# Performance work log

Hardware: AMD Instinct MI355X
Metric: run time of the kernel (lower is better)

## Reference

```python
import jax, jax.numpy as jnp
import numpy as np

R, S, N, D_IN, D_OUT = 4, 8, 4096, 64, 64


def prelu(v, alpha):
    # torch.nn.PReLU with a single learnable slope (default init 0.25)
    return jnp.where(v >= 0, v, alpha * v)


def setup_inputs() -> dict:
    key = jax.random.key(0)
    ks = jax.random.split(key, 6)
    theta = jax.random.uniform(ks[0], (R, S), dtype=jnp.float32)
    t = jax.random.uniform(ks[1], (R, S), dtype=jnp.float32)
    a = jax.random.uniform(ks[2], (R, N, N), dtype=jnp.float32)
    x = jax.random.normal(ks[3], (R, N, D_IN), dtype=jnp.float32)
    # per-relation Linear(input_dim, output_dim): weight [out,in], bias [out]
    fc_w = jax.random.normal(ks[4], (R, D_OUT, D_IN), dtype=jnp.float32) * (1.0 / np.sqrt(D_IN))
    fc_b = jnp.zeros((R, D_OUT), dtype=jnp.float32)
    # Conv2d(R, R, kernel_size=1): weight [R,R,1,1] -> [R,R], bias [R]
    conv_w = jax.random.normal(ks[5], (R, R), dtype=jnp.float32) * (1.0 / np.sqrt(R))
    conv_b = jnp.zeros((R,), dtype=jnp.float32)
    alpha0 = jnp.array(0.25, dtype=jnp.float32)  # PReLU for per-relation activation
    alpha1 = jnp.array(0.25, dtype=jnp.float32)  # PReLU after 1x1 conv
    return dict(theta=theta, t=t, a=a, x=x, fc_w=fc_w, fc_b=fc_b,
                conv_w=conv_w, conv_b=conv_b, alpha0=alpha0, alpha1=alpha1)


def reference(theta, t, a, x, fc_w, fc_b, conv_w, conv_b, alpha0, alpha1):
    # sum_step theta[r,s]*t[r,s]*a[r] == (sum_s theta[r,s]*t[r,s]) * a[r]
    coef = jnp.sum(theta * t, axis=-1)                               # [R]
    # diffusion: scaled dense matmul per relation (scale after matmul to avoid
    # materializing a scaled copy of the NxN matrix)
    feat = coef[:, None, None] * jnp.einsum('rij,rjd->rid', a, x)    # [R,N,D_IN]
    # per-relation Linear + PReLU
    diffusions = prelu(jnp.einsum('rnd,rod->rno', feat, fc_w) + fc_b[:, None, :], alpha0)  # [R,N,D_OUT]
    # 1x1 Conv2d over relation channels + PReLU
    latent = prelu(jnp.einsum('sr,rno->sno', conv_w, diffusions) + conv_b[:, None, None], alpha1)
    return (latent, diffusions)
```

## Files before the change

kernel.cpp:

```cpp
#include <hip/hip_runtime.h>

#define R_ 4
#define S_ 8
#define N_ 4096
#define D_ 64
#define KS_ 128
#define NST_ (N_ / KS_)

typedef __attribute__((ext_vector_type(8))) short bf16x8;
typedef __attribute__((ext_vector_type(4))) float f32x4;

__device__ __forceinline__ unsigned short f2bf(float f) {
    unsigned int u = __float_as_uint(f);
    u = (u + 0x7FFFu + ((u >> 16) & 1u)) >> 16;
    return (unsigned short)u;
}

__device__ __forceinline__ bf16x8 packbf(float4 u, float4 v) {
    bf16x8 f;
    f[0] = (short)f2bf(u.x); f[1] = (short)f2bf(u.y);
    f[2] = (short)f2bf(u.z); f[3] = (short)f2bf(u.w);
    f[4] = (short)f2bf(v.x); f[5] = (short)f2bf(v.y);
    f[6] = (short)f2bf(v.z); f[7] = (short)f2bf(v.w);
    return f;
}

__global__ __launch_bounds__(256) void prep_kernel(
    const float* __restrict__ theta, const float* __restrict__ tt,
    const float* __restrict__ x, const float* __restrict__ fc_w,
    unsigned short* __restrict__ ycombT) {
    int r  = blockIdx.x >> 6;
    int kb = blockIdx.x & 63;
    int tid = threadIdx.x;

    __shared__ float xs[64][64];
    __shared__ float ws[64][65];

    const float* xp = x    + ((size_t)r * N_ + (size_t)kb * 64) * D_;
    const float* wp = fc_w + (size_t)r * D_ * D_;
    for (int i = 0; i < 16; ++i) {
        int flat = i * 256 + tid;
        xs[flat >> 6][flat & 63] = xp[flat];
        ws[flat >> 6][flat & 63] = wp[flat];
    }
    float coef = 0.f;
#pragma unroll
    for (int s = 0; s < S_; ++s) coef += theta[r * S_ + s] * tt[r * S_ + s];
    __syncthreads();

    int o = tid & 63, kg = tid >> 6;
    for (int kl = kg; kl < 64; kl += 4) {
        float dot = 0.f;
#pragma unroll
        for (int d = 0; d < D_; ++d) dot += xs[kl][d] * ws[o][d];
        ycombT[(size_t)(r * D_ + o) * N_ + (size_t)kb * 64 + kl] = f2bf(coef * dot);
    }
}

__global__ __launch_bounds__(512) void gemm_kernel(
    const float* __restrict__ a, const unsigned short* __restrict__ ycombT,
    const float* __restrict__ fc_b, const float* __restrict__ alpha0p,
    float* __restrict__ out) {
    int bid = blockIdx.x;
    int r   = bid & 3;
    int rb  = bid >> 2;
    int tid  = threadIdx.x;
    int wave = tid >> 6;
    int wm   = wave & 3;
    int wk   = wave >> 2;
    int lane = tid & 63;
    int l15  = lane & 15;
    int kg   = lane >> 4;

    __shared__ __align__(16) unsigned short bs[2][64][KS_];
    __shared__ float red[4][16][65];

    int srow = tid >> 3, g2 = (tid & 7) * 2;
    int swz  = (srow & 7) << 1;
    const unsigned short* ysrc = ycombT + (size_t)(r * D_ + srow) * N_ + g2 * 8;

    const float* arow = a + ((size_t)(r * N_ + rb * 64 + wm * 16 + l15)) * N_
                          + wk * 64 + kg * 8;

    f32x4 acc0 = {0.f, 0.f, 0.f, 0.f};
    f32x4 acc1 = {0.f, 0.f, 0.f, 0.f};
    f32x4 acc2 = {0.f, 0.f, 0.f, 0.f};
    f32x4 acc3 = {0.f, 0.f, 0.f, 0.f};

    int swzr = (l15 & 7) << 1;
    int sl0 = ((wk * 8 + 0 + kg) ^ swzr) * 8;
    int sl1 = ((wk * 8 + 4 + kg) ^ swzr) * 8;

    float4 ac0 = *(const float4*)(arow + 0);
    float4 ac1 = *(const float4*)(arow + 4);
    float4 ac2 = *(const float4*)(arow + 32);
    float4 ac3 = *(const float4*)(arow + 36);
    uint4 bv0 = *(const uint4*)(ysrc);
    uint4 bv1 = *(const uint4*)(ysrc + 8);
    *(uint4*)&bs[0][srow][((g2    ) ^ swz) * 8] = bv0;
    *(uint4*)&bs[0][srow][((g2 + 1) ^ swz) * 8] = bv1;
    __syncthreads();
    bv0 = *(const uint4*)(ysrc + KS_);
    bv1 = *(const uint4*)(ysrc + KS_ + 8);
    float4 an0 = *(const float4*)(arow + KS_ + 0);
    float4 an1 = *(const float4*)(arow + KS_ + 4);
    float4 an2 = *(const float4*)(arow + KS_ + 32);
    float4 an3 = *(const float4*)(arow + KS_ + 36);

    for (int s = 0; s < NST_; ++s) {
        int buf = s & 1;
        bf16x8 af0 = packbf(ac0, ac1);
        bf16x8 af1 = packbf(ac2, ac3);
        bf16x8 b00 = *(const bf16x8*)&bs[buf][ 0 + l15][sl0];
        bf16x8 b10 = *(const bf16x8*)&bs[buf][16 + l15][sl0];
        bf16x8 b20 = *(const bf16x8*)&bs[buf][32 + l15][sl0];
        bf16x8 b30 = *(const bf16x8*)&bs[buf][48 + l15][sl0];
        acc0 = __builtin_amdgcn_mfma_f32_16x16x32_bf16(af0, b00, acc0, 0, 0, 0);
        acc1 = __builtin_amdgcn_mfma_f32_16x16x32_bf16(af0, b10, acc1, 0, 0, 0);
        acc2 = __builtin_amdgcn_mfma_f32_16x16x32_bf16(af0, b20, acc2, 0, 0, 0);
        acc3 = __builtin_amdgcn_mfma_f32_16x16x32_bf16(af0, b30, acc3, 0, 0, 0);
        bf16x8 b01 = *(const bf16x8*)&bs[buf][ 0 + l15][sl1];
        bf16x8 b11 = *(const bf16x8*)&bs[buf][16 + l15][sl1];
        bf16x8 b21 = *(const bf16x8*)&bs[buf][32 + l15][sl1];
        bf16x8 b31 = *(const bf16x8*)&bs[buf][48 + l15][sl1];
        acc0 = __builtin_amdgcn_mfma_f32_16x16x32_bf16(af1, b01, acc0, 0, 0, 0);
        acc1 = __builtin_amdgcn_mfma_f32_16x16x32_bf16(af1, b11, acc1, 0, 0, 0);
        acc2 = __builtin_amdgcn_mfma_f32_16x16x32_bf16(af1, b21, acc2, 0, 0, 0);
        acc3 = __builtin_amdgcn_mfma_f32_16x16x32_bf16(af1, b31, acc3, 0, 0, 0);

        ac0 = an0; ac1 = an1; ac2 = an2; ac3 = an3;
        if (s + 2 < NST_) {
            an0 = *(const float4*)(arow + (size_t)(s + 2) * KS_ + 0);
            an1 = *(const float4*)(arow + (size_t)(s + 2) * KS_ + 4);
            an2 = *(const float4*)(arow + (size_t)(s + 2) * KS_ + 32);
            an3 = *(const float4*)(arow + (size_t)(s + 2) * KS_ + 36);
        }
        __syncthreads();
        if (s + 1 < NST_) {
            *(uint4*)&bs[buf ^ 1][srow][((g2    ) ^ swz) * 8] = bv0;
            *(uint4*)&bs[buf ^ 1][srow][((g2 + 1) ^ swz) * 8] = bv1;
            if (s + 2 < NST_) {
                bv0 = *(const uint4*)(ysrc + (size_t)(s + 2) * KS_);
                bv1 = *(const uint4*)(ysrc + (size_t)(s + 2) * KS_ + 8);
            }
            __syncthreads();
        }
    }

    if (wk == 1) {
#pragma unroll
        for (int c = 0; c < 4; ++c) {
            f32x4 acc = (c == 0) ? acc0 : (c == 1) ? acc1 : (c == 2) ? acc2 : acc3;
#pragma unroll
            for (int j = 0; j < 4; ++j)
                red[wm][kg * 4 + j][c * 16 + l15] = acc[j];
        }
    }
    __syncthreads();
    if (wk == 0) {
        const float alpha0 = *alpha0p;
        const size_t diff_off = (size_t)R_ * N_ * D_;
#pragma unroll
        for (int c = 0; c < 4; ++c) {
            f32x4 acc = (c == 0) ? acc0 : (c == 1) ? acc1 : (c == 2) ? acc2 : acc3;
            int col = c * 16 + l15;
            float b = fc_b[r * D_ + col];
#pragma unroll
            for (int j = 0; j < 4; ++j) {
                int rloc = kg * 4 + j;
                float v = acc[j] + red[wm][rloc][col] + b;
                v = (v >= 0.f) ? v : alpha0 * v;
                out[diff_off + ((size_t)(r * N_ + rb * 64 + wm * 16 + rloc)) * D_ + col] = v;
            }
        }
    }
}

__global__ __launch_bounds__(256) void conv_kernel(
    const float* __restrict__ conv_w, const float* __restrict__ conv_b,
    const float* __restrict__ alpha1p, float* __restrict__ out) {
    const size_t nd = (size_t)N_ * D_;
    const size_t diff_off = (size_t)R_ * nd;
    size_t i = ((size_t)blockIdx.x * 256 + threadIdx.x) * 4;

    float4 d0 = *(const float4*)(out + diff_off + 0 * nd + i);
    float4 d1 = *(const float4*)(out + diff_off + 1 * nd + i);
    float4 d2 = *(const float4*)(out + diff_off + 2 * nd + i);
    float4 d3 = *(const float4*)(out + diff_off + 3 * nd + i);
    const float alpha1 = *alpha1p;
#pragma unroll
    for (int s = 0; s < R_; ++s) {
        float w0 = conv_w[s * R_ + 0], w1 = conv_w[s * R_ + 1];
        float w2 = conv_w[s * R_ + 2], w3 = conv_w[s * R_ + 3];
        float cb = conv_b[s];
        float4 v;
        v.x = cb + w0 * d0.x + w1 * d1.x + w2 * d2.x + w3 * d3.x;
        v.y = cb + w0 * d0.y + w1 * d1.y + w2 * d2.y + w3 * d3.y;
        v.z = cb + w0 * d0.z + w1 * d1.z + w2 * d2.z + w3 * d3.z;
        v.w = cb + w0 * d0.w + w1 * d1.w + w2 * d2.w + w3 * d3.w;
        v.x = (v.x >= 0.f) ? v.x : alpha1 * v.x;
        v.y = (v.y >= 0.f) ? v.y : alpha1 * v.y;
        v.z = (v.z >= 0.f) ? v.z : alpha1 * v.z;
        v.w = (v.w >= 0.f) ? v.w : alpha1 * v.w;
        *(float4*)(out + s * nd + i) = v;
    }
}

extern "C" void kernel_launch(void* const* d_in, const int* in_sizes, int n_in,
                              void* d_out, int out_size, void* d_ws, size_t ws_size,
                              hipStream_t stream) {
    const float* theta  = (const float*)d_in[0];
    const float* tt     = (const float*)d_in[1];
    const float* a      = (const float*)d_in[2];
    const float* x      = (const float*)d_in[3];
    const float* fc_w   = (const float*)d_in[4];
    const float* fc_b   = (const float*)d_in[5];
    const float* conv_w = (const float*)d_in[6];
    const float* conv_b = (const float*)d_in[7];
    const float* alpha0 = (const float*)d_in[8];
    const float* alpha1 = (const float*)d_in[9];
    float* out = (float*)d_out;
    unsigned short* ycombT = (unsigned short*)d_ws;

    prep_kernel<<<dim3(R_ * (N_ / 64)), dim3(256), 0, stream>>>(theta, tt, x, fc_w, ycombT);
    gemm_kernel<<<dim3((N_ / 64) * R_), dim3(512), 0, stream>>>(a, ycombT, fc_b, alpha0, out);
    conv_kernel<<<dim3((N_ * D_) / 4 / 256), dim3(256), 0, stream>>>(conv_w, conv_b, alpha1, out);
}
```

Before: 70.59 us.

## Split-K the A@Y GEMM into four partials and fuse reduction with conv epilogue

```diff
diff --git a/kernel.cpp b/kernel.cpp
--- a/kernel.cpp
+++ b/kernel.cpp
@@ -5,7 +5,9 @@
 #define N_ 4096
 #define D_ 64
 #define KS_ 128
-#define NST_ (N_ / KS_)
+#define KQ_ 1024
+#define NST_ (KQ_ / KS_)
+#define PART_ELEMS ((size_t)4 * R_ * N_ * D_)
 
 typedef __attribute__((ext_vector_type(8))) short bf16x8;
 typedef __attribute__((ext_vector_type(4))) float f32x4;
@@ -57,83 +59,101 @@
     }
 }
 
-__global__ __launch_bounds__(512) void gemm_kernel(
+__global__ __launch_bounds__(512, 2) void gemm_kernel(
     const float* __restrict__ a, const unsigned short* __restrict__ ycombT,
-    const float* __restrict__ fc_b, const float* __restrict__ alpha0p,
-    float* __restrict__ out) {
+    float* __restrict__ part) {
     int bid = blockIdx.x;
     int r   = bid & 3;
-    int rb  = bid >> 2;
+    int q   = (bid >> 2) & 3;
+    int rg  = bid >> 4;
     int tid  = threadIdx.x;
     int wave = tid >> 6;
-    int wm   = wave & 3;
-    int wk   = wave >> 2;
     int lane = tid & 63;
     int l15  = lane & 15;
     int kg   = lane >> 4;
 
     __shared__ __align__(16) unsigned short bs[2][64][KS_];
-    __shared__ float red[4][16][65];
 
     int srow = tid >> 3, g2 = (tid & 7) * 2;
     int swz  = (srow & 7) << 1;
-    const unsigned short* ysrc = ycombT + (size_t)(r * D_ + srow) * N_ + g2 * 8;
-
-    const float* arow = a + ((size_t)(r * N_ + rb * 64 + wm * 16 + l15)) * N_
-                          + wk * 64 + kg * 8;
-
-    f32x4 acc0 = {0.f, 0.f, 0.f, 0.f};
-    f32x4 acc1 = {0.f, 0.f, 0.f, 0.f};
-    f32x4 acc2 = {0.f, 0.f, 0.f, 0.f};
-    f32x4 acc3 = {0.f, 0.f, 0.f, 0.f};
+    const unsigned short* ysrc =
+        ycombT + (size_t)(r * D_ + srow) * N_ + (size_t)q * KQ_ + g2 * 8;
+
+    const float* ar0 = a + ((size_t)(r * N_ + rg * 256 + wave * 32 + l15)) * N_
+                         + (size_t)q * KQ_ + kg * 8;
+    const float* ar1 = ar0 + (size_t)16 * N_;
+
+    f32x4 acc[2][4];
+#pragma unroll
+    for (int st = 0; st < 2; ++st)
+#pragma unroll
+        for (int o = 0; o < 4; ++o) acc[st][o] = (f32x4){0.f, 0.f, 0.f, 0.f};
 
     int swzr = (l15 & 7) << 1;
-    int sl0 = ((wk * 8 + 0 + kg) ^ swzr) * 8;
-    int sl1 = ((wk * 8 + 4 + kg) ^ swzr) * 8;
-
-    float4 ac0 = *(const float4*)(arow + 0);
-    float4 ac1 = *(const float4*)(arow + 4);
-    float4 ac2 = *(const float4*)(arow + 32);
-    float4 ac3 = *(const float4*)(arow + 36);
-    uint4 bv0 = *(const uint4*)(ysrc);
-    uint4 bv1 = *(const uint4*)(ysrc + 8);
+
+    float4 an[2][8];
+    bf16x8 af[2][4];
+    uint4 bv0, bv1;
+
+#pragma unroll
+    for (int c = 0; c < 4; ++c) {
+        an[0][2 * c]     = *(const float4*)(ar0 + c * 32);
+        an[0][2 * c + 1] = *(const float4*)(ar0 + c * 32 + 4);
+        an[1][2 * c]     = *(const float4*)(ar1 + c * 32);
+        an[1][2 * c + 1] = *(const float4*)(ar1 + c * 32 + 4);
+    }
+    bv0 = *(const uint4*)(ysrc);
+    bv1 = *(const uint4*)(ysrc + 8);
     *(uint4*)&bs[0][srow][((g2    ) ^ swz) * 8] = bv0;
     *(uint4*)&bs[0][srow][((g2 + 1) ^ swz) * 8] = bv1;
-    __syncthreads();
+#pragma unroll
+    for (int st = 0; st < 2; ++st)
+#pragma unroll
+        for (int c = 0; c < 4; ++c)
+            af[st][c] = packbf(an[st][2 * c], an[st][2 * c + 1]);
+#pragma unroll
+    for (int c = 0; c < 4; ++c) {
+        an[0][2 * c]     = *(const float4*)(ar0 + KS_ + c * 32);
+        an[0][2 * c + 1] = *(const float4*)(ar0 + KS_ + c * 32 + 4);
+        an[1][2 * c]     = *(const float4*)(ar1 + KS_ + c * 32);
+        an[1][2 * c + 1] = *(const float4*)(ar1 + KS_ + c * 32 + 4);
+    }
     bv0 = *(const uint4*)(ysrc + KS_);
     bv1 = *(const uint4*)(ysrc + KS_ + 8);
-    float4 an0 = *(const float4*)(arow + KS_ + 0);
-    float4 an1 = *(const float4*)(arow + KS_ + 4);
-    float4 an2 = *(const float4*)(arow + KS_ + 32);
-    float4 an3 = *(const float4*)(arow + KS_ + 36);
+    __syncthreads();
 
     for (int s = 0; s < NST_; ++s) {
         int buf = s & 1;
-        bf16x8 af0 = packbf(ac0, ac1);
-        bf16x8 af1 = packbf(ac2, ac3);
-        bf16x8 b00 = *(const bf16x8*)&bs[buf][ 0 + l15][sl0];
-        bf16x8 b10 = *(const bf16x8*)&bs[buf][16 + l15][sl0];
-        bf16x8 b20 = *(const bf16x8*)&bs[buf][32 + l15][sl0];
-        bf16x8 b30 = *(const bf16x8*)&bs[buf][48 + l15][sl0];
-        acc0 = __builtin_amdgcn_mfma_f32_16x16x32_bf16(af0, b00, acc0, 0, 0, 0);
-        acc1 = __builtin_amdgcn_mfma_f32_16x16x32_bf16(af0, b10, acc1, 0, 0, 0);
-        acc2 = __builtin_amdgcn_mfma_f32_16x16x32_bf16(af0, b20, acc2, 0, 0, 0);
-        acc3 = __builtin_amdgcn_mfma_f32_16x16x32_bf16(af0, b30, acc3, 0, 0, 0);
-        bf16x8 b01 = *(const bf16x8*)&bs[buf][ 0 + l15][sl1];
-        bf16x8 b11 = *(const bf16x8*)&bs[buf][16 + l15][sl1];
-        bf16x8 b21 = *(const bf16x8*)&bs[buf][32 + l15][sl1];
-        bf16x8 b31 = *(const bf16x8*)&bs[buf][48 + l15][sl1];
-        acc0 = __builtin_amdgcn_mfma_f32_16x16x32_bf16(af1, b01, acc0, 0, 0, 0);
-        acc1 = __builtin_amdgcn_mfma_f32_16x16x32_bf16(af1, b11, acc1, 0, 0, 0);
-        acc2 = __builtin_amdgcn_mfma_f32_16x16x32_bf16(af1, b21, acc2, 0, 0, 0);
-        acc3 = __builtin_amdgcn_mfma_f32_16x16x32_bf16(af1, b31, acc3, 0, 0, 0);
-
-        ac0 = an0; ac1 = an1; ac2 = an2; ac3 = an3;
+#pragma unroll
+        for (int c = 0; c < 4; ++c) {
+            int sl = ((c * 4 + kg) ^ swzr) * 8;
+            bf16x8 b0 = *(const bf16x8*)&bs[buf][ 0 + l15][sl];
+            bf16x8 b1 = *(const bf16x8*)&bs[buf][16 + l15][sl];
+            bf16x8 b2 = *(const bf16x8*)&bs[buf][32 + l15][sl];
+            bf16x8 b3 = *(const bf16x8*)&bs[buf][48 + l15][sl];
+            acc[0][0] = __builtin_amdgcn_mfma_f32_16x16x32_bf16(af[0][c], b0, acc[0][0], 0, 0, 0);
+            acc[0][1] = __builtin_amdgcn_mfma_f32_16x16x32_bf16(af[0][c], b1, acc[0][1], 0, 0, 0);
+            acc[0][2] = __builtin_amdgcn_mfma_f32_16x16x32_bf16(af[0][c], b2, acc[0][2], 0, 0, 0);
+            acc[0][3] = __builtin_amdgcn_mfma_f32_16x16x32_bf16(af[0][c], b3, acc[0][3], 0, 0, 0);
+            acc[1][0] = __builtin_amdgcn_mfma_f32_16x16x32_bf16(af[1][c], b0, acc[1][0], 0, 0, 0);
+            acc[1][1] = __builtin_amdgcn_mfma_f32_16x16x32_bf16(af[1][c], b1, acc[1][1], 0, 0, 0);
+            acc[1][2] = __builtin_amdgcn_mfma_f32_16x16x32_bf16(af[1][c], b2, acc[1][2], 0, 0, 0);
+            acc[1][3] = __builtin_amdgcn_mfma_f32_16x16x32_bf16(af[1][c], b3, acc[1][3], 0, 0, 0);
+        }
+#pragma unroll
+        for (int st = 0; st < 2; ++st)
+#pragma unroll
+            for (int c = 0; c < 4; ++c)
+                af[st][c] = packbf(an[st][2 * c], an[st][2 * c + 1]);
         if (s + 2 < NST_) {
-            an0 = *(const float4*)(arow + (size_t)(s + 2) * KS_ + 0);
-            an1 = *(const float4*)(arow + (size_t)(s + 2) * KS_ + 4);
-            an2 = *(const float4*)(arow + (size_t)(s + 2) * KS_ + 32);
-            an3 = *(const float4*)(arow + (size_t)(s + 2) * KS_ + 36);
+            size_t ko = (size_t)(s + 2) * KS_;
+#pragma unroll
+            for (int c = 0; c < 4; ++c) {
+                an[0][2 * c]     = *(const float4*)(ar0 + ko + c * 32);
+                an[0][2 * c + 1] = *(const float4*)(ar0 + ko + c * 32 + 4);
+                an[1][2 * c]     = *(const float4*)(ar1 + ko + c * 32);
+                an[1][2 * c + 1] = *(const float4*)(ar1 + ko + c * 32 + 4);
+            }
         }
         __syncthreads();
         if (s + 1 < NST_) {
@@ -147,62 +167,60 @@
         }
     }
 
-    if (wk == 1) {
-#pragma unroll
-        for (int c = 0; c < 4; ++c) {
-            f32x4 acc = (c == 0) ? acc0 : (c == 1) ? acc1 : (c == 2) ? acc2 : acc3;
+    float* pb = part + (((size_t)(q * R_ + r) * N_) + rg * 256 + wave * 32) * D_;
+#pragma unroll
+    for (int st = 0; st < 2; ++st)
+#pragma unroll
+        for (int c = 0; c < 4; ++c)
 #pragma unroll
             for (int j = 0; j < 4; ++j)
-                red[wm][kg * 4 + j][c * 16 + l15] = acc[j];
-        }
-    }
-    __syncthreads();
-    if (wk == 0) {
-        const float alpha0 = *alpha0p;
-        const size_t diff_off = (size_t)R_ * N_ * D_;
-#pragma unroll
-        for (int c = 0; c < 4; ++c) {
-            f32x4 acc = (c == 0) ? acc0 : (c == 1) ? acc1 : (c == 2) ? acc2 : acc3;
-            int col = c * 16 + l15;
-            float b = fc_b[r * D_ + col];
-#pragma unroll
-            for (int j = 0; j < 4; ++j) {
-                int rloc = kg * 4 + j;
-                float v = acc[j] + red[wm][rloc][col] + b;
-                v = (v >= 0.f) ? v : alpha0 * v;
-                out[diff_off + ((size_t)(r * N_ + rb * 64 + wm * 16 + rloc)) * D_ + col] = v;
-            }
-        }
-    }
-}
-
-__global__ __launch_bounds__(256) void conv_kernel(
+                pb[(size_t)(st * 16 + kg * 4 + j) * D_ + c * 16 + l15] = acc[st][c][j];
+}
+
+__global__ __launch_bounds__(256) void combine_kernel(
+    const float* __restrict__ part, const float* __restrict__ fc_b,
     const float* __restrict__ conv_w, const float* __restrict__ conv_b,
-    const float* __restrict__ alpha1p, float* __restrict__ out) {
+    const float* __restrict__ alpha0p, const float* __restrict__ alpha1p,
+    float* __restrict__ out) {
     const size_t nd = (size_t)N_ * D_;
     const size_t diff_off = (size_t)R_ * nd;
     size_t i = ((size_t)blockIdx.x * 256 + threadIdx.x) * 4;
-
-    float4 d0 = *(const float4*)(out + diff_off + 0 * nd + i);
-    float4 d1 = *(const float4*)(out + diff_off + 1 * nd + i);
-    float4 d2 = *(const float4*)(out + diff_off + 2 * nd + i);
-    float4 d3 = *(const float4*)(out + diff_off + 3 * nd + i);
-    const float alpha1 = *alpha1p;
-#pragma unroll
-    for (int s = 0; s < R_; ++s) {
-        float w0 = conv_w[s * R_ + 0], w1 = conv_w[s * R_ + 1];
-        float w2 = conv_w[s * R_ + 2], w3 = conv_w[s * R_ + 3];
-        float cb = conv_b[s];
+    int col0 = (int)(i & 63);
+    const float alpha0 = *alpha0p, alpha1 = *alpha1p;
+
+    float4 diff[4];
+#pragma unroll
+    for (int r = 0; r < R_; ++r) {
+        float4 s = {0.f, 0.f, 0.f, 0.f};
+#pragma unroll
+        for (int qq = 0; qq < 4; ++qq) {
+            float4 p = *(const float4*)(part + (size_t)(qq * R_ + r) * nd + i);
+            s.x += p.x; s.y += p.y; s.z += p.z; s.w += p.w;
+        }
+        float4 b = *(const float4*)(fc_b + r * D_ + col0);
+        s.x += b.x; s.y += b.y; s.z += b.z; s.w += b.w;
+        s.x = (s.x >= 0.f) ? s.x : alpha0 * s.x;
+        s.y = (s.y >= 0.f) ? s.y : alpha0 * s.y;
+        s.z = (s.z >= 0.f) ? s.z : alpha0 * s.z;
+        s.w = (s.w >= 0.f) ? s.w : alpha0 * s.w;
+        diff[r] = s;
+        *(float4*)(out + diff_off + r * nd + i) = s;
+    }
+#pragma unroll
+    for (int sx = 0; sx < R_; ++sx) {
+        float w0 = conv_w[sx * R_ + 0], w1 = conv_w[sx * R_ + 1];
+        float w2 = conv_w[sx * R_ + 2], w3 = conv_w[sx * R_ + 3];
+        float cb = conv_b[sx];
         float4 v;
-        v.x = cb + w0 * d0.x + w1 * d1.x + w2 * d2.x + w3 * d3.x;
-        v.y = cb + w0 * d0.y + w1 * d1.y + w2 * d2.y + w3 * d3.y;
-        v.z = cb + w0 * d0.z + w1 * d1.z + w2 * d2.z + w3 * d3.z;
-        v.w = cb + w0 * d0.w + w1 * d1.w + w2 * d2.w + w3 * d3.w;
+        v.x = cb + w0 * diff[0].x + w1 * diff[1].x + w2 * diff[2].x + w3 * diff[3].x;
+        v.y = cb + w0 * diff[0].y + w1 * diff[1].y + w2 * diff[2].y + w3 * diff[3].y;
+        v.z = cb + w0 * diff[0].z + w1 * diff[1].z + w2 * diff[2].z + w3 * diff[3].z;
+        v.w = cb + w0 * diff[0].w + w1 * diff[1].w + w2 * diff[2].w + w3 * diff[3].w;
         v.x = (v.x >= 0.f) ? v.x : alpha1 * v.x;
         v.y = (v.y >= 0.f) ? v.y : alpha1 * v.y;
         v.z = (v.z >= 0.f) ? v.z : alpha1 * v.z;
         v.w = (v.w >= 0.f) ? v.w : alpha1 * v.w;
-        *(float4*)(out + s * nd + i) = v;
+        *(float4*)(out + sx * nd + i) = v;
     }
 }
 
@@ -220,9 +238,13 @@
     const float* alpha0 = (const float*)d_in[8];
     const float* alpha1 = (const float*)d_in[9];
     float* out = (float*)d_out;
-    unsigned short* ycombT = (unsigned short*)d_ws;
+
+    float* part = (float*)d_ws;
+    unsigned short* ycombT =
+        (unsigned short*)((char*)d_ws + PART_ELEMS * sizeof(float));
 
     prep_kernel<<<dim3(R_ * (N_ / 64)), dim3(256), 0, stream>>>(theta, tt, x, fc_w, ycombT);
-    gemm_kernel<<<dim3((N_ / 64) * R_), dim3(512), 0, stream>>>(a, ycombT, fc_b, alpha0, out);
-    conv_kernel<<<dim3((N_ * D_) / 4 / 256), dim3(256), 0, stream>>>(conv_w, conv_b, alpha1, out);
-}
+    gemm_kernel<<<dim3(256), dim3(512), 0, stream>>>(a, ycombT, part);
+    combine_kernel<<<dim3((N_ * D_) / 4 / 256), dim3(256), 0, stream>>>(
+        part, fc_b, conv_w, conv_b, alpha0, alpha1, out);
+}
```

New measurement: 71.59 us. No clear change (+1.4%).

## Stage A tiles through shared memory as bf16 with coalesced row loads

Applied to the files above, without the earlier changes.

```diff
diff --git a/kernel.cpp b/kernel.cpp
--- a/kernel.cpp
+++ b/kernel.cpp
@@ -10,19 +10,9 @@
 typedef __attribute__((ext_vector_type(8))) short bf16x8;
 typedef __attribute__((ext_vector_type(4))) float f32x4;
 
-__device__ __forceinline__ unsigned short f2bf(float f) {
+__device__ __forceinline__ unsigned int f2bf(float f) {
     unsigned int u = __float_as_uint(f);
-    u = (u + 0x7FFFu + ((u >> 16) & 1u)) >> 16;
-    return (unsigned short)u;
-}
-
-__device__ __forceinline__ bf16x8 packbf(float4 u, float4 v) {
-    bf16x8 f;
-    f[0] = (short)f2bf(u.x); f[1] = (short)f2bf(u.y);
-    f[2] = (short)f2bf(u.z); f[3] = (short)f2bf(u.w);
-    f[4] = (short)f2bf(v.x); f[5] = (short)f2bf(v.y);
-    f[6] = (short)f2bf(v.z); f[7] = (short)f2bf(v.w);
-    return f;
+    return (u + 0x7FFFu + ((u >> 16) & 1u)) >> 16;
 }
 
 __global__ __launch_bounds__(256) void prep_kernel(
@@ -53,7 +43,8 @@
         float dot = 0.f;
 #pragma unroll
         for (int d = 0; d < D_; ++d) dot += xs[kl][d] * ws[o][d];
-        ycombT[(size_t)(r * D_ + o) * N_ + (size_t)kb * 64 + kl] = f2bf(coef * dot);
+        ycombT[(size_t)(r * D_ + o) * N_ + (size_t)kb * 64 + kl] =
+            (unsigned short)f2bf(coef * dot);
     }
 }
 
@@ -72,81 +63,90 @@
     int l15  = lane & 15;
     int kg   = lane >> 4;
 
-    __shared__ __align__(16) unsigned short bs[2][64][KS_];
-    __shared__ float red[4][16][65];
+    __shared__ __align__(16) char pool[65536];
+#define ABASE(buf) ((buf) * 16384)
+#define BBASE(buf) (32768 + (buf) * 16384)
+
+    int arow_loc = tid >> 5;
+    int ak       = (tid & 31) * 4;
+    int agran    = (tid & 31) >> 1;
+    int ahalf    = tid & 1;
+    int swzA     = (arow_loc & 7) << 1;
+    const float* asrc = a + ((size_t)(r * N_ + rb * 64)) * N_;
 
     int srow = tid >> 3, g2 = (tid & 7) * 2;
-    int swz  = (srow & 7) << 1;
+    int swzB = (srow & 7) << 1;
     const unsigned short* ysrc = ycombT + (size_t)(r * D_ + srow) * N_ + g2 * 8;
 
-    const float* arow = a + ((size_t)(r * N_ + rb * 64 + wm * 16 + l15)) * N_
-                          + wk * 64 + kg * 8;
+    int swzr = (l15 & 7) << 1;
 
     f32x4 acc0 = {0.f, 0.f, 0.f, 0.f};
     f32x4 acc1 = {0.f, 0.f, 0.f, 0.f};
     f32x4 acc2 = {0.f, 0.f, 0.f, 0.f};
     f32x4 acc3 = {0.f, 0.f, 0.f, 0.f};
 
-    int swzr = (l15 & 7) << 1;
-    int sl0 = ((wk * 8 + 0 + kg) ^ swzr) * 8;
-    int sl1 = ((wk * 8 + 4 + kg) ^ swzr) * 8;
-
-    float4 ac0 = *(const float4*)(arow + 0);
-    float4 ac1 = *(const float4*)(arow + 4);
-    float4 ac2 = *(const float4*)(arow + 32);
-    float4 ac3 = *(const float4*)(arow + 36);
-    uint4 bv0 = *(const uint4*)(ysrc);
-    uint4 bv1 = *(const uint4*)(ysrc + 8);
-    *(uint4*)&bs[0][srow][((g2    ) ^ swz) * 8] = bv0;
-    *(uint4*)&bs[0][srow][((g2 + 1) ^ swz) * 8] = bv1;
+    float4 an[4];
+    uint4  bv0, bv1;
+
+    auto loadA = [&](int s) {
+#pragma unroll
+        for (int j = 0; j < 4; ++j)
+            an[j] = *(const float4*)(asrc + (size_t)(j * 16 + arow_loc) * N_
+                                          + (size_t)s * KS_ + ak);
+    };
+    auto loadB = [&](int s) {
+        bv0 = *(const uint4*)(ysrc + (size_t)s * KS_);
+        bv1 = *(const uint4*)(ysrc + (size_t)s * KS_ + 8);
+    };
+    auto writeA = [&](int buf) {
+#pragma unroll
+        for (int j = 0; j < 4; ++j) {
+            int rowj = j * 16 + arow_loc;
+            uint2 p;
+            p.x = (f2bf(an[j].y) << 16) | f2bf(an[j].x);
+            p.y = (f2bf(an[j].w) << 16) | f2bf(an[j].z);
+            *(uint2*)(pool + ABASE(buf) + rowj * 256
+                      + ((agran ^ swzA) << 4) + (ahalf << 3)) = p;
+        }
+    };
+    auto writeB = [&](int buf) {
+        *(uint4*)(pool + BBASE(buf) + srow * 256 + (((g2    ) ^ swzB) << 4)) = bv0;
+        *(uint4*)(pool + BBASE(buf) + srow * 256 + (((g2 + 1) ^ swzB) << 4)) = bv1;
+    };
+    auto compute = [&](int buf) {
+#pragma unroll
+        for (int step = 0; step < 2; ++step) {
+            int slot = (((wk * 8 + step * 4 + kg) ^ swzr)) << 4;
+            bf16x8 af = *(const bf16x8*)(pool + ABASE(buf) + (wm * 16 + l15) * 256 + slot);
+            bf16x8 b0 = *(const bf16x8*)(pool + BBASE(buf) + ( 0 + l15) * 256 + slot);
+            bf16x8 b1 = *(const bf16x8*)(pool + BBASE(buf) + (16 + l15) * 256 + slot);
+            bf16x8 b2 = *(const bf16x8*)(pool + BBASE(buf) + (32 + l15) * 256 + slot);
+            bf16x8 b3 = *(const bf16x8*)(pool + BBASE(buf) + (48 + l15) * 256 + slot);
+            acc0 = __builtin_amdgcn_mfma_f32_16x16x32_bf16(af, b0, acc0, 0, 0, 0);
+            acc1 = __builtin_amdgcn_mfma_f32_16x16x32_bf16(af, b1, acc1, 0, 0, 0);
+            acc2 = __builtin_amdgcn_mfma_f32_16x16x32_bf16(af, b2, acc2, 0, 0, 0);
+            acc3 = __builtin_amdgcn_mfma_f32_16x16x32_bf16(af, b3, acc3, 0, 0, 0);
+        }
+    };
+
+    loadA(0); loadB(0);
+    writeA(0); writeB(0);
+    loadA(1); loadB(1);
     __syncthreads();
-    bv0 = *(const uint4*)(ysrc + KS_);
-    bv1 = *(const uint4*)(ysrc + KS_ + 8);
-    float4 an0 = *(const float4*)(arow + KS_ + 0);
-    float4 an1 = *(const float4*)(arow + KS_ + 4);
-    float4 an2 = *(const float4*)(arow + KS_ + 32);
-    float4 an3 = *(const float4*)(arow + KS_ + 36);
-
+
+#pragma unroll 2
     for (int s = 0; s < NST_; ++s) {
         int buf = s & 1;
-        bf16x8 af0 = packbf(ac0, ac1);
-        bf16x8 af1 = packbf(ac2, ac3);
-        bf16x8 b00 = *(const bf16x8*)&bs[buf][ 0 + l15][sl0];
-        bf16x8 b10 = *(const bf16x8*)&bs[buf][16 + l15][sl0];
-        bf16x8 b20 = *(const bf16x8*)&bs[buf][32 + l15][sl0];
-        bf16x8 b30 = *(const bf16x8*)&bs[buf][48 + l15][sl0];
-        acc0 = __builtin_amdgcn_mfma_f32_16x16x32_bf16(af0, b00, acc0, 0, 0, 0);
-        acc1 = __builtin_amdgcn_mfma_f32_16x16x32_bf16(af0, b10, acc1, 0, 0, 0);
-        acc2 = __builtin_amdgcn_mfma_f32_16x16x32_bf16(af0, b20, acc2, 0, 0, 0);
-        acc3 = __builtin_amdgcn_mfma_f32_16x16x32_bf16(af0, b30, acc3, 0, 0, 0);
-        bf16x8 b01 = *(const bf16x8*)&bs[buf][ 0 + l15][sl1];
-        bf16x8 b11 = *(const bf16x8*)&bs[buf][16 + l15][sl1];
-        bf16x8 b21 = *(const bf16x8*)&bs[buf][32 + l15][sl1];
-        bf16x8 b31 = *(const bf16x8*)&bs[buf][48 + l15][sl1];
-        acc0 = __builtin_amdgcn_mfma_f32_16x16x32_bf16(af1, b01, acc0, 0, 0, 0);
-        acc1 = __builtin_amdgcn_mfma_f32_16x16x32_bf16(af1, b11, acc1, 0, 0, 0);
-        acc2 = __builtin_amdgcn_mfma_f32_16x16x32_bf16(af1, b21, acc2, 0, 0, 0);
-        acc3 = __builtin_amdgcn_mfma_f32_16x16x32_bf16(af1, b31, acc3, 0, 0, 0);
-
-        ac0 = an0; ac1 = an1; ac2 = an2; ac3 = an3;
-        if (s + 2 < NST_) {
-            an0 = *(const float4*)(arow + (size_t)(s + 2) * KS_ + 0);
-            an1 = *(const float4*)(arow + (size_t)(s + 2) * KS_ + 4);
-            an2 = *(const float4*)(arow + (size_t)(s + 2) * KS_ + 32);
-            an3 = *(const float4*)(arow + (size_t)(s + 2) * KS_ + 36);
-        }
+        compute(buf);
         __syncthreads();
         if (s + 1 < NST_) {
-            *(uint4*)&bs[buf ^ 1][srow][((g2    ) ^ swz) * 8] = bv0;
-            *(uint4*)&bs[buf ^ 1][srow][((g2 + 1) ^ swz) * 8] = bv1;
-            if (s + 2 < NST_) {
-                bv0 = *(const uint4*)(ysrc + (size_t)(s + 2) * KS_);
-                bv1 = *(const uint4*)(ysrc + (size_t)(s + 2) * KS_ + 8);
-            }
+            writeA(buf ^ 1); writeB(buf ^ 1);
+            if (s + 2 < NST_) { loadA(s + 2); loadB(s + 2); }
             __syncthreads();
         }
     }
 
+    float (*red)[16][65] = (float (*)[16][65])pool;
     if (wk == 1) {
 #pragma unroll
         for (int c = 0; c < 4; ++c) {
```

Result: faster. 59.37 us, median of 2 (-15.9%).
